# Optimization experiments

Hardware: AMD Instinct MI355X
Metric: run time of the kernel (lower is better)

The kernel has to match this reference:

```python
import jax, jax.numpy as jnp
import numpy as np
from jax import lax

B, C, L, G = 2048, 9605, 20, 50
ALPHA, ALPHA1, ALPHA2, ALPHA3, ALPHA_OTHER = 0.5, 0.05, 2.0, 10.0, 0.5
NEG_INF = jnp.float32(-1e30)


def setup_inputs() -> dict:
    k0, k1, k2, k3 = jax.random.split(jax.random.key(0), 4)
    x = jax.random.normal(k0, (B, C), jnp.float32)
    # sparse multi-label targets (~10 positives/row) so at most ~1 whitelist group is active,
    # matching the original code's assert len(gt_whitelist_index) == 1
    y = (jax.random.uniform(k1, (B, C)) < 0.001).astype(jnp.int32)
    y_neg = (jax.random.uniform(k2, (B, C)) < 0.001).astype(jnp.int32)
    # L disjoint whitelist groups of G classes each (from mapping_dict in the original)
    idx = jax.random.permutation(k3, C)[: L * G].reshape(L, G)
    group_mask = jnp.zeros((L, C), bool).at[jnp.arange(L)[:, None], idx].set(True)
    return {"x": x, "y": y, "y_neg": y_neg, "group_mask": group_mask}


def _rank_loss(x1, x2, margin):
    # our_rank_loss: sigmoid(alpha3*(x2-x1+margin)), scaled by alpha2 when positive
    d = x2 - x1 + margin
    s = jax.nn.sigmoid(ALPHA3 * d)
    return jnp.where(d > 0, ALPHA2 * s, s)


def reference(x, y, y_neg, group_mask):
    xs = jax.nn.sigmoid(x)  # [B, C]
    gmf = group_mask.astype(jnp.float32)  # [L, C]

    # per-row max score inside each whitelist group -> [B, L]
    # lax.map over the L (=20) groups keeps peak memory at one [B, C] temp per step
    group_max = lax.map(
        lambda m: jnp.max(jnp.where(m, xs, NEG_INF), axis=-1), group_mask
    ).T  # [B, L]

    # find_gt_whitelist: group k active iff sum(y[group_k]) > 0
    active = jnp.einsum("bc,lc->bl", y.astype(jnp.float32), gmf) > 0
    active_neg = jnp.einsum("bc,lc->bl", y_neg.astype(jnp.float32), gmf) > 0
    has_gt = jnp.any(active, axis=-1)  # [B]
    g = jnp.argmax(active, axis=-1)  # first active group (original asserts exactly one)

    # top_k_thres = max(11th largest sigmoid score, alpha_other) in both branches
    thres = jnp.maximum(lax.top_k(xs, 11)[0][:, 10], ALPHA_OTHER)  # [B]

    # max over union of all whitelist classes (wl_indices)
    union_max = jnp.max(jnp.where(jnp.any(group_mask, 0)[None, :], xs, NEG_INF), -1)

    gt_max = jnp.take_along_axis(group_max, g[:, None], axis=1)[:, 0]  # [B]
    # incorrect_max: max(0, max over groups != g); incorrect_neg: max(0, max over neg-active groups)
    excl = jnp.where(jnp.arange(L)[None, :] == g[:, None], NEG_INF, group_max)
    incorrect_max = jnp.maximum(jnp.max(excl, -1), 0.0)
    incorrect_neg = jnp.maximum(jnp.max(jnp.where(active_neg, group_max, 0.0), -1), 0.0)

    # branch A: no gt whitelist group active
    case_a = (1 - ALPHA) * _rank_loss(thres, union_max, ALPHA1) + ALPHA * _rank_loss(
        thres, incorrect_neg, ALPHA1
    )
    # branch B: exactly one gt group g
    case_b = (
        _rank_loss(gt_max, thres, ALPHA1)
        + jnp.where(
            incorrect_max > 0, (1 - ALPHA) * _rank_loss(thres, incorrect_max, ALPHA1), 0.0
        )
        + jnp.where(
            incorrect_neg > 0,
            ALPHA * _rank_loss(thres, incorrect_neg, ALPHA1),
            ALPHA * _rank_loss(thres, incorrect_max, ALPHA1),
        )
    )
    return jnp.sum(jnp.where(has_gt, case_b, case_a))
```

## Files before the change

kernel.cpp:

```cpp
#include <hip/hip_runtime.h>
#include <stdint.h>

#define B_ROWS 2048
#define C_CLS  9605
#define L_GRP  20
#define GM_BYTES (L_GRP * C_CLS)
#define REPSTRIDE 9728
#define LIST_OFF  39040
#define LIST_CAP  16384
#define NEG_BIG -3.0e38f

__device__ __forceinline__ float sigmoidf(float v) {
  return 1.0f / (1.0f + __expf(-v));
}

__device__ __forceinline__ float rank_loss(float x1, float x2) {
  float d = x2 - x1 + 0.05f;
  float s = 1.0f / (1.0f + __expf(-10.0f * d));
  return d > 0.0f ? 2.0f * s : s;
}

__device__ __forceinline__ unsigned fmap(float f) {
  unsigned u = __float_as_uint(f);
  return (u & 0x80000000u) ? ~u : (u | 0x80000000u);
}
__device__ __forceinline__ float funmap(unsigned m) {
  unsigned u = (m & 0x80000000u) ? (m ^ 0x80000000u) : ~m;
  return __uint_as_float(u);
}

#define INS1(ti) { float hi = fmaxf(ti, a); a = fminf(ti, a); ti = hi; }
#define INSERT(v)                                                         \
  do {                                                                    \
    if ((v) > t10) {                                                      \
      float a = (v);                                                      \
      INS1(t0) INS1(t1) INS1(t2) INS1(t3) INS1(t4) INS1(t5) INS1(t6)      \
      INS1(t7) INS1(t8) INS1(t9) INS1(t10)                                \
    }                                                                     \
  } while (0)

#define PROC(av, wv)                                                          \
  do {                                                                        \
    const float m4_ = fmaxf(fmaxf(av.x, av.y), fmaxf(av.z, av.w));            \
    if (m4_ > t10) { INSERT(av.x); INSERT(av.y); INSERT(av.z); INSERT(av.w); }\
    if ((wv) != 0xFFFFFFFFu) {                                                \
      const unsigned q0_ = (wv) & 0xFFu, q1_ = ((wv) >> 8) & 0xFFu,           \
                     q2_ = ((wv) >> 16) & 0xFFu, q3_ = (wv) >> 24;            \
      if (q0_ < L_GRP) atomicMax(&s_gmax[q0_], fmap(av.x));                   \
      if (q1_ < L_GRP) atomicMax(&s_gmax[q1_], fmap(av.y));                   \
      if (q2_ < L_GRP) atomicMax(&s_gmax[q2_], fmap(av.z));                   \
      if (q3_ < L_GRP) atomicMax(&s_gmax[q3_], fmap(av.w));                   \
    }                                                                         \
  } while (0)

__global__ void probe_init_kernel(const uint4* __restrict__ gm,
                                  unsigned char* __restrict__ ws,
                                  float* __restrict__ out) {
  __shared__ int s_part[16];
  const int tid = threadIdx.x;
  if (tid == 0) {
    out[0] = 0.0f;
    ((int*)ws)[1] = 0;
  }
  for (int i = tid; i < 4 * REPSTRIDE; i += 1024) ws[64 + i] = 0xFF;
  int local = 0;
  const int nvec = GM_BYTES / 16;
  for (int i = tid; i < nvec; i += 1024) {
    uint4 w = gm[i];
    unsigned a[4] = {w.x, w.y, w.z, w.w};
#pragma unroll
    for (int q = 0; q < 4; ++q) {
      local += ((a[q] & 0x000000FFu) != 0) + ((a[q] & 0x0000FF00u) != 0) +
               ((a[q] & 0x00FF0000u) != 0) + ((a[q] & 0xFF000000u) != 0);
    }
  }
  if (tid == 0) {
    const unsigned char* gb = (const unsigned char*)gm;
    for (int i = nvec * 16; i < GM_BYTES; ++i) local += (gb[i] != 0);
  }
#pragma unroll
  for (int off = 32; off; off >>= 1) local += __shfl_xor(local, off);
  if ((tid & 63) == 0) s_part[tid >> 6] = local;
  __syncthreads();
  if (tid == 0) {
    int tot = 0;
    for (int w = 0; w < 16; ++w) tot += s_part[w];
    ((int*)ws)[0] = tot;
  }
}

__global__ void build_gid_kernel(const void* gm, unsigned char* __restrict__ ws) {
  int i = blockIdx.x * blockDim.x + threadIdx.x;
  if (i >= GM_BYTES) return;
  const bool is_byte = (((const int*)ws)[0] > 600);
  bool m;
  if (is_byte) m = ((const unsigned char*)gm)[i] != 0;
  else         m = ((const unsigned int*)gm)[i] != 0u;
  if (m) {
    int l = i / C_CLS;
    int c = i - l * C_CLS;
    unsigned char* base = ws + 64;
#pragma unroll
    for (int r = 0; r < 4; ++r) base[r * REPSTRIDE + r + c] = (unsigned char)l;
    int slot = atomicAdd(&((int*)ws)[1], 1);
    if (slot < LIST_CAP) ((int*)(ws + LIST_OFF))[slot] = c | (l << 16);
  }
}

__global__ __launch_bounds__(256, 8) void loss_kernel(
    const float* __restrict__ x, const int* __restrict__ y,
    const int* __restrict__ yn, const unsigned char* __restrict__ ws,
    float* __restrict__ out) {
  __shared__ unsigned s_gmax[L_GRP];
  __shared__ unsigned s_act, s_actn;
  __shared__ float s_wtop[4 * 11];
  const int tid = threadIdx.x;
  const int lane = tid & 63;
  const int wave = tid >> 6;
  const int row = blockIdx.x;

  const size_t base = (size_t)row * C_CLS;
  const int mis = (int)(base & 3);
  const int peel = (4 - mis) & 3;
  const float* xr = x + base;
  const int* yr = y + base;
  const int* nr = yn + base;
  const unsigned char* gidc = ws + 64 + mis * REPSTRIDE + mis;

  if (tid < L_GRP) s_gmax[tid] = 0u;
  if (tid == 0) { s_act = 0u; s_actn = 0u; }
  __syncthreads();

  float t0 = NEG_BIG, t1 = NEG_BIG, t2 = NEG_BIG, t3 = NEG_BIG, t4 = NEG_BIG,
        t5 = NEG_BIG, t6 = NEG_BIG, t7 = NEG_BIG, t8 = NEG_BIG, t9 = NEG_BIG,
        t10 = NEG_BIG;

  if (tid < peel) {
    float v = xr[tid];
    INSERT(v);
    unsigned gk = gidc[tid];
    if (gk < L_GRP) atomicMax(&s_gmax[gk], fmap(v));
  }

  const int nvec = (C_CLS - peel) >> 2;
  const float4* x4 = (const float4*)(xr + peel);
  const unsigned* g4 = (const unsigned*)(gidc + peel);

  for (int jb = tid; jb < nvec; jb += 1024) {
    const int j1 = jb + 256, j2 = jb + 512, j3 = jb + 768;
    const bool k1 = j1 < nvec, k2 = j2 < nvec, k3 = j3 < nvec;
    float4 a0 = x4[jb];
    float4 a1 = x4[k1 ? j1 : jb];
    float4 a2 = x4[k2 ? j2 : jb];
    float4 a3 = x4[k3 ? j3 : jb];
    unsigned w0 = g4[jb];
    unsigned w1 = k1 ? g4[j1] : 0xFFFFFFFFu;
    unsigned w2 = k2 ? g4[j2] : 0xFFFFFFFFu;
    unsigned w3 = k3 ? g4[j3] : 0xFFFFFFFFu;
    if (!k1) a1.x = a1.y = a1.z = a1.w = NEG_BIG;
    if (!k2) a2.x = a2.y = a2.z = a2.w = NEG_BIG;
    if (!k3) a3.x = a3.y = a3.z = a3.w = NEG_BIG;
    PROC(a0, w0);
    PROC(a1, w1);
    PROC(a2, w2);
    PROC(a3, w3);
  }

  const int tail0 = peel + (nvec << 2);
  if (tid < C_CLS - tail0) {
    const int c = tail0 + tid;
    float v = xr[c];
    INSERT(v);
    unsigned gk = gidc[c];
    if (gk < L_GRP) atomicMax(&s_gmax[gk], fmap(v));
  }

  {
    const int cntr = ((const int*)ws)[1];
    const int n = cntr < LIST_CAP ? cntr : LIST_CAP;
    const int* list = (const int*)(ws + LIST_OFF);
    unsigned aL = 0u, anL = 0u;
#pragma unroll
    for (int k = 0; k < 4; ++k) {
      const int i = tid + k * 256;
      const bool ok = i < n;
      const int e = list[ok ? i : 0];
      const int c = e & 0xFFFF;
      const unsigned bit = ok ? (1u << (e >> 16)) : 0u;
      if (yr[c] != 0) aL |= bit;
      if (nr[c] != 0) anL |= bit;
    }
    for (int i = tid + 1024; i < n; i += 256) {
      const int e = list[i];
      const int c = e & 0xFFFF;
      const unsigned bit = 1u << (e >> 16);
      if (yr[c] != 0) aL |= bit;
      if (nr[c] != 0) anL |= bit;
    }
    if (aL) atomicOr(&s_act, aL);
    if (anL) atomicOr(&s_actn, anL);
  }

  float cur = t0;
  float mr[11];
#pragma unroll
  for (int r = 0; r < 11; ++r) {
    float m = cur;
#pragma unroll
    for (int off = 32; off; off >>= 1) m = fmaxf(m, __shfl_xor(m, off));
    mr[r] = m;
    if (r < 10) {
      unsigned long long b = __ballot(cur == m);
      int leader = (int)(__ffsll(b) - 1);
      if (lane == leader) {
        t0 = t1; t1 = t2; t2 = t3; t3 = t4; t4 = t5; t5 = t6; t6 = t7;
        t7 = t8; t8 = t9; t9 = t10; t10 = NEG_BIG;
        cur = t0;
      }
    }
  }
  if (lane == 0) {
#pragma unroll
    for (int r = 0; r < 11; ++r) s_wtop[wave * 11 + r] = mr[r];
  }
  __syncthreads();

  if (wave == 0) {
    float v = (lane < 44) ? s_wtop[lane] : NEG_BIG;
    float eleventh = NEG_BIG;
#pragma unroll
    for (int r = 0; r < 11; ++r) {
      float m = v;
#pragma unroll
      for (int off = 32; off; off >>= 1) m = fmaxf(m, __shfl_xor(m, off));
      eleventh = m;
      if (r < 10) {
        unsigned long long b = __ballot(v == m);
        int leader = (int)(__ffsll(b) - 1);
        if (lane == leader) v = NEG_BIG;
      }
    }

    const unsigned aL = s_act, anL = s_actn;
    const bool has_gt = (aL != 0u);
    const int g = has_gt ? (__ffs(aL) - 1) : 0;
    const float thres = fmaxf(sigmoidf(eleventh), 0.5f);

    float union_max = NEG_BIG, gt_sg = 0.0f, inc_max = NEG_BIG, inc_neg = 0.0f;
#pragma unroll
    for (int l = 0; l < L_GRP; ++l) {
      float sg = sigmoidf(funmap(s_gmax[l]));
      union_max = fmaxf(union_max, sg);
      if (l == g) gt_sg = sg; else inc_max = fmaxf(inc_max, sg);
      if ((anL >> l) & 1u) inc_neg = fmaxf(inc_neg, sg);
    }
    inc_max = fmaxf(inc_max, 0.0f);
    inc_neg = fmaxf(inc_neg, 0.0f);

    float loss;
    if (has_gt) {
      loss = rank_loss(gt_sg, thres);
      if (inc_max > 0.0f) loss += 0.5f * rank_loss(thres, inc_max);
      loss += 0.5f * rank_loss(thres, (inc_neg > 0.0f) ? inc_neg : inc_max);
    } else {
      loss = 0.5f * rank_loss(thres, union_max) + 0.5f * rank_loss(thres, inc_neg);
    }
    if (lane == 0) atomicAdd(out, loss);
  }
}

extern "C" void kernel_launch(void* const* d_in, const int* in_sizes, int n_in,
                              void* d_out, int out_size, void* d_ws, size_t ws_size,
                              hipStream_t stream) {
  (void)in_sizes; (void)n_in; (void)out_size; (void)ws_size;
  const float* x = (const float*)d_in[0];
  const int* y = (const int*)d_in[1];
  const int* yn = (const int*)d_in[2];
  const void* gm = d_in[3];

  unsigned char* ws = (unsigned char*)d_ws;

  probe_init_kernel<<<1, 1024, 0, stream>>>((const uint4*)gm, ws, (float*)d_out);
  build_gid_kernel<<<(GM_BYTES + 255) / 256, 256, 0, stream>>>(gm, ws);
  loss_kernel<<<B_ROWS, 256, 0, stream>>>(x, y, yn, ws, (float*)d_out);
}
```

Baseline: 257.6 us.

## Stream row scores through double-buffered LDS via async global-to-LDS loads

Replaces the per-thread strided float4 loads of each score row with asynchronous global_load_lds transfers into a two-slot shared-memory buffer of 512 float4s. The next chunk is issued while the current one is processed, separated by a block barrier per chunk. The goal is to overlap global memory latency with the top-k and group-max work. In exchange it adds 16 KB of LDS per block and a barrier per chunk, and each thread has fewer independent loads in flight than the previous 4-way unrolled loop.

```diff
diff --git a/kernel.cpp b/kernel.cpp
--- a/kernel.cpp
+++ b/kernel.cpp
@@ -8,7 +8,11 @@
 #define REPSTRIDE 9728
 #define LIST_OFF  39040
 #define LIST_CAP  16384
+#define CHUNK 512
 #define NEG_BIG -3.0e38f
+
+typedef __attribute__((address_space(1))) const void global_cv;
+typedef __attribute__((address_space(3))) void lds_v;
 
 __device__ __forceinline__ float sigmoidf(float v) {
   return 1.0f / (1.0f + __expf(-v));
@@ -111,6 +115,7 @@
     const float* __restrict__ x, const int* __restrict__ y,
     const int* __restrict__ yn, const unsigned char* __restrict__ ws,
     float* __restrict__ out) {
+  __shared__ float4 s_x[2][CHUNK];
   __shared__ unsigned s_gmax[L_GRP];
   __shared__ unsigned s_act, s_actn;
   __shared__ float s_wtop[4 * 11];
@@ -142,31 +147,42 @@
     if (gk < L_GRP) atomicMax(&s_gmax[gk], fmap(v));
   }
 
-  const int nvec = (C_CLS - peel) >> 2;
+  const int NV = (C_CLS - peel) >> 2;
   const float4* x4 = (const float4*)(xr + peel);
   const unsigned* g4 = (const unsigned*)(gidc + peel);
 
-  for (int jb = tid; jb < nvec; jb += 1024) {
-    const int j1 = jb + 256, j2 = jb + 512, j3 = jb + 768;
-    const bool k1 = j1 < nvec, k2 = j2 < nvec, k3 = j3 < nvec;
-    float4 a0 = x4[jb];
-    float4 a1 = x4[k1 ? j1 : jb];
-    float4 a2 = x4[k2 ? j2 : jb];
-    float4 a3 = x4[k3 ? j3 : jb];
-    unsigned w0 = g4[jb];
-    unsigned w1 = k1 ? g4[j1] : 0xFFFFFFFFu;
-    unsigned w2 = k2 ? g4[j2] : 0xFFFFFFFFu;
-    unsigned w3 = k3 ? g4[j3] : 0xFFFFFFFFu;
-    if (!k1) a1.x = a1.y = a1.z = a1.w = NEG_BIG;
-    if (!k2) a2.x = a2.y = a2.z = a2.w = NEG_BIG;
-    if (!k3) a3.x = a3.y = a3.z = a3.w = NEG_BIG;
+  auto issue = [&](int cbase, int b) {
+    const int cend = (cbase + CHUNK < NV) ? cbase + CHUNK : NV;
+#pragma unroll
+    for (int r = 0; r < 2; ++r) {
+      const int j = cbase + r * 256 + tid;
+      if (j < cend) {
+        __builtin_amdgcn_global_load_lds(
+            (global_cv*)(x4 + j),
+            (lds_v*)&s_x[b][r * 256 + (tid & ~63)], 16, 0, 0);
+      }
+    }
+  };
+
+  const int nchunks = (NV + CHUNK - 1) / CHUNK;
+  issue(0, 0);
+  for (int c = 0; c < nchunks; ++c) {
+    __syncthreads();
+    if (c + 1 < nchunks) issue((c + 1) * CHUNK, (c + 1) & 1);
+    const int cbase = c * CHUNK;
+    const int csz = (NV - cbase < CHUNK) ? NV - cbase : CHUNK;
+    const float4* sb = s_x[c & 1];
+    const bool k0 = tid < csz, k1 = tid + 256 < csz;
+    unsigned w0 = k0 ? g4[cbase + tid] : 0xFFFFFFFFu;
+    unsigned w1 = k1 ? g4[cbase + tid + 256] : 0xFFFFFFFFu;
+    float4 a0, a1;
+    if (k0) a0 = sb[tid]; else a0.x = a0.y = a0.z = a0.w = NEG_BIG;
+    if (k1) a1 = sb[tid + 256]; else a1.x = a1.y = a1.z = a1.w = NEG_BIG;
     PROC(a0, w0);
     PROC(a1, w1);
-    PROC(a2, w2);
-    PROC(a3, w3);
-  }
-
-  const int tail0 = peel + (nvec << 2);
+  }
+
+  const int tail0 = peel + (NV << 2);
   if (tid < C_CLS - tail0) {
     const int c = tail0 + tid;
     float v = xr[c];
```

Measured after the change: 259.8 us. About the same (+0.8%).

## Prefilter top-11 candidates by fixed threshold into shared survivor list

Applied to the files above, without the earlier changes.

Drops the per-thread 11-register insertion sort from the main streaming loop. Values above a fixed threshold of 2.0 are now appended to a shared-memory survivor list with an atomic counter. After a barrier, each thread inserts only the survivors into its local top-11. If fewer than 11 or more than the capacity survive, it rescans the whole row from global memory. This makes the hot loop cheaper and lightens register pressure, at the cost of shared atomics and an extra sync. It relies on the input distribution so that the fallback path stays rare.

```diff
diff --git a/kernel.cpp b/kernel.cpp
--- a/kernel.cpp
+++ b/kernel.cpp
@@ -8,6 +8,8 @@
 #define REPSTRIDE 9728
 #define LIST_OFF  39040
 #define LIST_CAP  16384
+#define FILT_T 2.0f
+#define SURV_CAP 768
 #define NEG_BIG -3.0e38f
 
 __device__ __forceinline__ float sigmoidf(float v) {
@@ -39,10 +41,18 @@
     }                                                                     \
   } while (0)
 
+#define SURV1(v)                                                          \
+  do {                                                                    \
+    if ((v) > FILT_T) {                                                   \
+      int ix_ = atomicAdd(&s_cnt, 1);                                     \
+      if (ix_ < SURV_CAP) s_surv[ix_] = (v);                              \
+    }                                                                     \
+  } while (0)
+
 #define PROC(av, wv)                                                          \
   do {                                                                        \
     const float m4_ = fmaxf(fmaxf(av.x, av.y), fmaxf(av.z, av.w));            \
-    if (m4_ > t10) { INSERT(av.x); INSERT(av.y); INSERT(av.z); INSERT(av.w); }\
+    if (m4_ > FILT_T) { SURV1(av.x); SURV1(av.y); SURV1(av.z); SURV1(av.w); } \
     if ((wv) != 0xFFFFFFFFu) {                                                \
       const unsigned q0_ = (wv) & 0xFFu, q1_ = ((wv) >> 8) & 0xFFu,           \
                      q2_ = ((wv) >> 16) & 0xFFu, q3_ = (wv) >> 24;            \
@@ -111,6 +121,8 @@
     const float* __restrict__ x, const int* __restrict__ y,
     const int* __restrict__ yn, const unsigned char* __restrict__ ws,
     float* __restrict__ out) {
+  __shared__ float s_surv[SURV_CAP];
+  __shared__ int s_cnt;
   __shared__ unsigned s_gmax[L_GRP];
   __shared__ unsigned s_act, s_actn;
   __shared__ float s_wtop[4 * 11];
@@ -128,16 +140,12 @@
   const unsigned char* gidc = ws + 64 + mis * REPSTRIDE + mis;
 
   if (tid < L_GRP) s_gmax[tid] = 0u;
-  if (tid == 0) { s_act = 0u; s_actn = 0u; }
+  if (tid == 0) { s_act = 0u; s_actn = 0u; s_cnt = 0; }
   __syncthreads();
-
-  float t0 = NEG_BIG, t1 = NEG_BIG, t2 = NEG_BIG, t3 = NEG_BIG, t4 = NEG_BIG,
-        t5 = NEG_BIG, t6 = NEG_BIG, t7 = NEG_BIG, t8 = NEG_BIG, t9 = NEG_BIG,
-        t10 = NEG_BIG;
 
   if (tid < peel) {
     float v = xr[tid];
-    INSERT(v);
+    SURV1(v);
     unsigned gk = gidc[tid];
     if (gk < L_GRP) atomicMax(&s_gmax[gk], fmap(v));
   }
@@ -170,7 +178,7 @@
   if (tid < C_CLS - tail0) {
     const int c = tail0 + tid;
     float v = xr[c];
-    INSERT(v);
+    SURV1(v);
     unsigned gk = gidc[c];
     if (gk < L_GRP) atomicMax(&s_gmax[gk], fmap(v));
   }
@@ -199,6 +207,22 @@
     }
     if (aL) atomicOr(&s_act, aL);
     if (anL) atomicOr(&s_actn, anL);
+  }
+
+  __syncthreads();
+
+  float t0 = NEG_BIG, t1 = NEG_BIG, t2 = NEG_BIG, t3 = NEG_BIG, t4 = NEG_BIG,
+        t5 = NEG_BIG, t6 = NEG_BIG, t7 = NEG_BIG, t8 = NEG_BIG, t9 = NEG_BIG,
+        t10 = NEG_BIG;
+  const int cnt = s_cnt;
+  if (cnt >= 11 && cnt <= SURV_CAP) {
+#pragma unroll
+    for (int k = 0; k < 3; ++k) {
+      const int i = tid + k * 256;
+      if (i < cnt) { float v = s_surv[i]; INSERT(v); }
+    }
+  } else {
+    for (int c = tid; c < C_CLS; c += 256) { float v = xr[c]; INSERT(v); }
   }
 
   float cur = t0;
```

Measured after the change: 259.1 us. About the same (+0.6%).
